# Optimization experiments

Hardware: AMD Instinct MI355X
Metric: run time of the kernel (lower is better)

## Reference

```python
import jax, jax.numpy as jnp
import numpy as np

N, E = 200_000, 1_000_000
WIDTH, NUM_HEAD = 128, 8
WN, WA = 1, 1            # width_norm, width_act
C = WIDTH * WN           # pre/norm channels
A = WIDTH * WA           # gate/value channels
BOND_SIZE, BAG = 33, 3
EPS = 1e-5               # GroupNorm eps (torch default)


def group_norm(x, groups, eps=EPS):
    # x: [E, C]; normalize per sample per group (affine=False, spatial size 1)
    e, c = x.shape
    xg = x.reshape(e, groups, c // groups)
    m = xg.mean(-1, keepdims=True)
    v = ((xg - m) ** 2).mean(-1, keepdims=True)
    return ((xg - m) * jax.lax.rsqrt(v + eps)).reshape(e, c)


def grouped1x1(x, w, groups):
    # grouped Conv1d with kernel 1, no bias. x: [E, Cin], w: [Cout, Cin//groups]
    e, cin = x.shape
    cout = w.shape[0]
    xg = x.reshape(e, groups, cin // groups)
    wg = w.reshape(groups, cout // groups, cin // groups)
    return jnp.einsum('egi,goi->ego', xg, wg).reshape(e, cout)


def setup_inputs() -> dict:
    key = jax.random.key(0)
    ks = jax.random.split(key, 12)
    x = jax.random.normal(ks[0], (N, WIDTH), jnp.float32)
    # degrees clamped to >= 1 in the original model
    deg = jnp.floor(jax.random.uniform(ks[1], (N,), jnp.float32, 1.0, 8.0))
    edge_idx = jax.random.randint(ks[2], (2, E), 0, N)
    edge_attr = jax.random.randint(ks[3], (E, BAG), 0, BOND_SIZE)
    s_in = 1.0 / np.sqrt(WIDTH)
    s_g = 1.0 / np.sqrt(C // NUM_HEAD)
    s_p = 1.0 / np.sqrt(A)
    pre0_w = jax.random.normal(ks[4], (C, WIDTH), jnp.float32) * s_in
    pre0_b = jnp.zeros((C,), jnp.float32)
    pre1_w = jax.random.normal(ks[5], (C, WIDTH), jnp.float32) * s_in
    pre1_b = jnp.zeros((C,), jnp.float32)
    emb = jax.random.normal(ks[6], (BOND_SIZE, C), jnp.float32)
    emb = emb.at[0].set(0.0)  # padding_idx=0
    gate_w = jax.random.normal(ks[7], (A, C // NUM_HEAD), jnp.float32) * s_g
    value_w = jax.random.normal(ks[8], (A, C // NUM_HEAD), jnp.float32) * s_g
    post_w = jax.random.normal(ks[9], (WIDTH, A), jnp.float32) * s_p
    post_b = jnp.zeros((WIDTH,), jnp.float32)
    degree_param = jnp.full((WIDTH,), -0.01, jnp.float32)
    return {"x": x, "deg": deg, "edge_idx": edge_idx, "edge_attr": edge_attr,
            "pre0_w": pre0_w, "pre0_b": pre0_b, "pre1_w": pre1_w, "pre1_b": pre1_b,
            "emb": emb, "gate_w": gate_w, "value_w": value_w,
            "post_w": post_w, "post_b": post_b, "degree_param": degree_param}


def reference(x, deg, edge_idx, edge_attr, pre0_w, pre0_b, pre1_w, pre1_b,
              emb, gate_w, value_w, post_w, post_b, degree_param):
    n = x.shape[0]
    # conv1x1 projections on nodes, then gather to edges
    h0 = x @ pre0_w.T + pre0_b                      # [N, C]
    h1 = x @ pre1_w.T + pre1_b                      # [N, C]
    xx = h0[edge_idx[0]] + h1[edge_idx[1]]          # [E, C]
    xx = group_norm(xx, NUM_HEAD)
    # EmbeddingBag mean with padding_idx=0 excluded from the mean
    mask = (edge_attr != 0)                          # [E, BAG]
    bag = (emb[edge_attr] * mask[..., None]).sum(1)  # [E, C]
    cnt = jnp.maximum(mask.sum(-1), 1).astype(xx.dtype)
    bag = bag / cnt[:, None]
    # GLU-style gate * value (Dropout is identity at eval)
    gate = jax.nn.relu(grouped1x1(xx + bag, gate_w, NUM_HEAD))  # [E, A]
    val = grouped1x1(xx, value_w, NUM_HEAD)                     # [E, A]
    xx = gate * val
    # scatter-sum back to destination nodes
    agg = jax.ops.segment_sum(xx, edge_idx[1], num_segments=n)  # [N, A]
    out = agg @ post_w.T + post_b                                # [N, WIDTH]
    out = jnp.power(deg[:, None], degree_param) * out
    return out
```

## Files before the change

### kernel.cpp

```cpp
#include <hip/hip_runtime.h>
#include <hip/hip_bf16.h>
#include <hip/hip_fp16.h>


typedef unsigned short u16;
typedef unsigned int   u32;

#define WIDTH 128

#define OFF_W0   0
#define OFF_B0   16384
#define OFF_W1   16512
#define OFF_B1   32896
#define OFF_EMB  33024
#define OFF_GW   37248
#define OFF_VW   39296
#define OFF_PW   41344
#define OFF_PB   57728
#define OFF_DP   57856
#define OFF_WGC  57984
#define OFF_WVC  74368
#define OFF_BGC  90752
#define OFF_BVC  90880
#define OFF_DEG  91008
#define ARENA_PAD 291072

typedef __attribute__((ext_vector_type(8))) short bf16x8;
typedef __attribute__((ext_vector_type(8))) _Float16 f16x8;
typedef __attribute__((ext_vector_type(4))) float f32x4;
typedef __attribute__((ext_vector_type(2))) __fp16 f16x2;

__device__ __forceinline__ float b2f(u16 u){ return __uint_as_float(((u32)u) << 16); }
__device__ __forceinline__ u16   f2b(float f){
  u32 u = __float_as_uint(f);
  u += 0x7fffu + ((u >> 16) & 1u);
  return (u16)(u >> 16);
}
__device__ __forceinline__ u16   f2h(float f){ return __half_as_ushort(__float2half(f)); }
__device__ __forceinline__ float h2f(u16 u){ return __half2float(__ushort_as_half(u)); }

__device__ __forceinline__ f16x2 u2h(u32 u){ union { u32 a; f16x2 b; } c; c.a = u; return c.b; }
__device__ __forceinline__ u32   h2u(f16x2 h){ union { f16x2 b; u32 a; } c; c.b = h; return c.a; }

__device__ __forceinline__ f16x2 pkhfma(f16x2 a, f16x2 b, f16x2 c){
#if __has_builtin(__builtin_elementwise_fma)
  return __builtin_elementwise_fma(a, b, c);
#else
  return a * b + c;
#endif
}

#define DPPADD(s, ctrl) {                                                  \
  const float _t = __uint_as_float((u32)__builtin_amdgcn_update_dpp(       \
      0, (int)__float_as_uint(s), (ctrl), 0xF, 0xF, true));                \
  (s) += _t; }

__device__ __forceinline__ bool is_fp32(const void* degsrc){
  return ((*(const u32*)degsrc) & 0xffffu) == 0u;
}

__device__ __forceinline__ bf16x8 cvt8(float4 a, float4 b){
  bf16x8 r;
  r[0]=(short)f2b(a.x); r[1]=(short)f2b(a.y); r[2]=(short)f2b(a.z); r[3]=(short)f2b(a.w);
  r[4]=(short)f2b(b.x); r[5]=(short)f2b(b.y); r[6]=(short)f2b(b.z); r[7]=(short)f2b(b.w);
  return r;
}
__device__ __forceinline__ f16x8 cvt8h(float4 a, float4 b){
  f16x8 r;
  r[0]=(_Float16)a.x; r[1]=(_Float16)a.y; r[2]=(_Float16)a.z; r[3]=(_Float16)a.w;
  r[4]=(_Float16)b.x; r[5]=(_Float16)b.y; r[6]=(_Float16)b.z; r[7]=(_Float16)b.w;
  return r;
}
__device__ __forceinline__ f16x8 cvtbh(bf16x8 v){
  f16x8 r;
  #pragma unroll
  for (int j = 0; j < 8; ++j) r[j] = (_Float16)b2f((u16)v[j]);
  return r;
}

__device__ __forceinline__ u16 cvt_one(const void* src, int j, bool f32){
  return f32 ? f2b(((const float*)src)[j]) : ((const u16*)src)[j];
}
__device__ __forceinline__ u16 cvt_one_h(const void* src, int j, bool f32){
  return f32 ? f2h(((const float*)src)[j]) : f2h(b2f(((const u16*)src)[j]));
}
__device__ __forceinline__ float read_f(const void* src, int j, bool f32){
  return f32 ? ((const float*)src)[j] : b2f(((const u16*)src)[j]);
}

__global__ void k_init_hist(const void* w0, const void* b0, const void* w1, const void* b1,
                            const void* emb, const void* gw, const void* vw,
                            const void* pw, const void* pb, const void* dp,
                            const void* degsrc, const int* __restrict__ eidx,
                            int* __restrict__ cnt, int E,
                            u16* __restrict__ pb16, u16* __restrict__ gembh,
                            float* __restrict__ gsums, int N)
{
  const bool f32 = is_fp32(degsrc);
  const int nbh = (E + 255) >> 8;
  const int tot_cvt = OFF_WGC + N;
  const int nbc = (tot_cvt + 255) >> 8;
  int b = blockIdx.x;
  const int t = threadIdx.x;

  if (b < nbh) {
    const int e = b * 256 + t;
    if (e < E) atomicAdd(&cnt[eidx[E + e]], 1);
    return;
  }
  b -= nbh;
  if (b < nbc) {
    const int i = b * 256 + t;
    if (i >= tot_cvt) return;
    u16 v; int dsti = i;
    if      (i < OFF_B0 ) v = cvt_one(w0,  i,           f32);
    else if (i < OFF_W1 ) v = cvt_one(b0,  i - OFF_B0,  f32);
    else if (i < OFF_B1 ) v = cvt_one(w1,  i - OFF_W1,  f32);
    else if (i < OFF_EMB) v = cvt_one(b1,  i - OFF_B1,  f32);
    else if (i < OFF_GW ) v = cvt_one(emb, i - OFF_EMB, f32);
    else if (i < OFF_VW ) v = cvt_one_h(gw, i - OFF_GW, f32);
    else if (i < OFF_PW ) v = cvt_one_h(vw, i - OFF_VW, f32);
    else if (i < OFF_PB ) v = cvt_one_h(pw, i - OFF_PW, f32);
    else if (i < OFF_DP ) v = cvt_one(pb,  i - OFF_PB,  f32);
    else if (i < OFF_WGC) v = cvt_one(dp,  i - OFF_DP,  f32);
    else { v = cvt_one(degsrc, i - OFF_WGC, f32); dsti = OFF_DEG + (i - OFF_WGC); }
    pb16[dsti] = v;
    return;
  }
  b -= nbc;
  if (b < 17) {
    const int tid = b * 256 + t;
    if (tid >= 33 * 128) return;
    const int a = tid >> 7, c = tid & 127, g = c >> 4;
    float s = 0.f;
    #pragma unroll
    for (int i = 0; i < 16; ++i)
      s += read_f(gw, c * 16 + i, f32) * read_f(emb, a * WIDTH + g * 16 + i, f32);
    gembh[tid] = f2h(s);
    return;
  }
  b -= 17;
  if (b < 1) {
    if (t < 256) {
      const int c = t & 127;
      const void* src = (t >> 7) ? vw : gw;
      float s = 0.f;
      #pragma unroll
      for (int i = 0; i < 16; ++i) s += read_f(src, c * 16 + i, f32);
      gsums[t] = s;
    }
    return;
  }
  b -= 1;
  if (b < 128) {
    const int tid = b * 256 + t;
    const int m = tid >> 14;
    const int o = (tid >> 7) & 127;
    const int i = tid & 127;
    const void* wsel = m ? vw : gw;
    const int hb = (o >> 4) * 16;
    float s = 0.f;
    #pragma unroll
    for (int j = 0; j < 16; ++j)
      s += read_f(wsel, o * 16 + j, f32) * read_f(w0, (size_t)(hb + j) * 128 + i, f32);
    pb16[(m ? OFF_WVC : OFF_WGC) + o * 128 + i] = f2h(s);
    return;
  }
  if (t < 256) {
    const int m = t >> 7, o = t & 127, hb = (o >> 4) * 16;
    const void* wsel = m ? vw : gw;
    float s = 0.f;
    #pragma unroll
    for (int j = 0; j < 16; ++j)
      s += read_f(wsel, o * 16 + j, f32) * read_f(b0, hb + j, f32);
    pb16[(m ? OFF_BVC : OFF_BGC) + o] = f2h(s);
  }
}

__global__ __launch_bounds__(512, 2) void k_pre_scan1(
    const void* __restrict__ x, const u16* __restrict__ pb16,
    u32* __restrict__ pk0ab, u32* __restrict__ uv0d, u32* __restrict__ h1d,
    const void* __restrict__ degsrc,
    const int* __restrict__ cnt, int* __restrict__ bsum, int n, int npre)
{
  if ((int)blockIdx.x >= npre) {
    const int t = threadIdx.x, b = (int)blockIdx.x - npre;
    const int i0 = b * 1024 + t * 2;
    int s = 0;
    if (i0     < n) s += cnt[i0];
    if (i0 + 1 < n) s += cnt[i0 + 1];
    __shared__ int sb[512];
    sb[t] = s; __syncthreads();
    for (int d = 256; d > 0; d >>= 1) { if (t < d) sb[t] += sb[t + d]; __syncthreads(); }
    if (t == 0) bsum[b] = sb[0];
    return;
  }

  const int t = threadIdx.x;
  const int lane = t & 63, lid = lane & 15, quad = lane >> 4;
  const int w = t >> 6, mat = w >> 1, c0 = (w & 1) * 64;
  const int node0 = blockIdx.x * 64;
  const bool f32 = is_fp32(degsrc);
  const bool hp16 = (mat == 1) || (mat == 2);

  const u16* wsrc; const u16* bsv;
  u32* outp; int slot = 0; bool pkmode = false;
  if      (mat == 0) { wsrc = pb16 + OFF_W0;  bsv = pb16 + OFF_B0;  outp = pk0ab; slot = 0; pkmode = true; }
  else if (mat == 1) { wsrc = pb16 + OFF_WGC; bsv = pb16 + OFF_BGC; outp = pk0ab; slot = 1; pkmode = true; }
  else if (mat == 2) { wsrc = pb16 + OFF_WVC; bsv = pb16 + OFF_BVC; outp = uv0d; }
  else               { wsrc = pb16 + OFF_W1;  bsv = pb16 + OFF_B1;  outp = h1d; }

  float bias[2][2];
  #pragma unroll
  for (int ntp = 0; ntp < 2; ++ntp)
    #pragma unroll
    for (int eo = 0; eo < 2; ++eo) {
      const u16 braw = bsv[c0 + ntp * 32 + 2 * lid + eo];
      bias[ntp][eo] = hp16 ? h2f(braw) : b2f(braw);
    }

  f32x4 acc[4][2][2];
  #pragma unroll
  for (int mt = 0; mt < 4; ++mt)
    #pragma unroll
    for (int ntp = 0; ntp < 2; ++ntp)
      #pragma unroll
      for (int eo = 0; eo < 2; ++eo)
        #pragma unroll
        for (int r = 0; r < 4; ++r) acc[mt][ntp][eo][r] = bias[ntp][eo];

  if (!hp16) {
    #pragma unroll
    for (int ks = 0; ks < 4; ++ks) {
      bf16x8 a[4], bb[2][2];
      #pragma unroll
      for (int ntp = 0; ntp < 2; ++ntp)
        #pragma unroll
        for (int eo = 0; eo < 2; ++eo)
          bb[ntp][eo] = *(const bf16x8*)(wsrc +
              (size_t)(c0 + ntp * 32 + 2 * lid + eo) * WIDTH + ks * 32 + quad * 8);
      if (f32) {
        #pragma unroll
        for (int mt = 0; mt < 4; ++mt) {
          const float4* xr = (const float4*)((const float*)x +
              (size_t)(node0 + mt * 16 + lid) * WIDTH + ks * 32 + quad * 8);
          a[mt] = cvt8(xr[0], xr[1]);
        }
      } else {
        #pragma unroll
        for (int mt = 0; mt < 4; ++mt)
          a[mt] = *(const bf16x8*)((const u16*)x +
              (size_t)(node0 + mt * 16 + lid) * WIDTH + ks * 32 + quad * 8);
      }
      #pragma unroll
      for (int mt = 0; mt < 4; ++mt)
        #pragma unroll
        for (int ntp = 0; ntp < 2; ++ntp)
          #pragma unroll
          for (int eo = 0; eo < 2; ++eo)
            acc[mt][ntp][eo] = __builtin_amdgcn_mfma_f32_16x16x32_bf16(
                a[mt], bb[ntp][eo], acc[mt][ntp][eo], 0, 0, 0);
    }
  } else {
    #pragma unroll
    for (int ks = 0; ks < 4; ++ks) {
      f16x8 a[4], bb[2][2];
      #pragma unroll
      for (int ntp = 0; ntp < 2; ++ntp)
        #pragma unroll
        for (int eo = 0; eo < 2; ++eo)
          bb[ntp][eo] = *(const f16x8*)(wsrc +
              (size_t)(c0 + ntp * 32 + 2 * lid + eo) * WIDTH + ks * 32 + quad * 8);
      if (f32) {
        #pragma unroll
        for (int mt = 0; mt < 4; ++mt) {
          const float4* xr = (const float4*)((const float*)x +
              (size_t)(node0 + mt * 16 + lid) * WIDTH + ks * 32 + quad * 8);
          a[mt] = cvt8h(xr[0], xr[1]);
        }
      } else {
        #pragma unroll
        for (int mt = 0; mt < 4; ++mt)
          a[mt] = cvtbh(*(const bf16x8*)((const u16*)x +
              (size_t)(node0 + mt * 16 + lid) * WIDTH + ks * 32 + quad * 8));
      }
      #pragma unroll
      for (int mt = 0; mt < 4; ++mt)
        #pragma unroll
        for (int ntp = 0; ntp < 2; ++ntp)
          #pragma unroll
          for (int eo = 0; eo < 2; ++eo)
            acc[mt][ntp][eo] = __builtin_amdgcn_mfma_f32_16x16x32_f16(
                a[mt], bb[ntp][eo], acc[mt][ntp][eo], 0, 0, 0);
    }
  }

  #pragma unroll
  for (int mt = 0; mt < 4; ++mt)
    #pragma unroll
    for (int r = 0; r < 4; ++r) {
      const int node = node0 + mt * 16 + quad * 4 + r;
      #pragma unroll
      for (int ntp = 0; ntp < 2; ++ntp) {
        const int p = (c0 >> 1) + ntp * 16 + lid;
        const u32 pk = h2u(__builtin_amdgcn_cvt_pkrtz(
            acc[mt][ntp][0][r], acc[mt][ntp][1][r]));
        if (pkmode) outp[(size_t)node * 128 + p * 2 + slot] = pk;
        else        outp[(size_t)node * 64 + p] = pk;
      }
    }
}

__global__ void k_scan3(const int* __restrict__ cnt, const int* __restrict__ bsum,
                        int* __restrict__ off, int n){
  const int t = threadIdx.x, b = blockIdx.x;
  __shared__ int sp[256];
  int pv = 0;
  for (int j = t; j < b; j += 256) pv += bsum[j];
  sp[t] = pv; __syncthreads();
  for (int d = 128; d > 0; d >>= 1) { if (t < d) sp[t] += sp[t + d]; __syncthreads(); }
  const int bpref = sp[0];

  const int i0 = b * 1024 + t * 4;
  int c[4];
  #pragma unroll
  for (int j = 0; j < 4; ++j) { int i = i0 + j; c[j] = (i < n) ? cnt[i] : 0; }
  int tsum = c[0] + c[1] + c[2] + c[3];
  __shared__ int sb[256];
  sb[t] = tsum; __syncthreads();
  for (int d = 1; d < 256; d <<= 1) {
    int x = (t >= d) ? sb[t - d] : 0;
    __syncthreads();
    sb[t] += x;
    __syncthreads();
  }
  int run = bpref + sb[t] - tsum;
  #pragma unroll
  for (int j = 0; j < 4; ++j) {
    int i = i0 + j;
    if (i < n) off[i] = run;
    run += c[j];
  }
}

__global__ void k_scatter(const int* __restrict__ eidx, const int* __restrict__ eattr,
                          int* __restrict__ off, uint2* __restrict__ sedge, int E){
  const int e = blockIdx.x * 256 + threadIdx.x;
  if (e >= E) return;
  const int dst = eidx[E + e];
  const int pos = atomicAdd(&off[dst], 1);
  const u32 a0 = (u32)eattr[e*3+0], a1 = (u32)eattr[e*3+1], a2 = (u32)eattr[e*3+2];
  u32 cb = (a0 != 0) + (a1 != 0) + (a2 != 0);
  cb = cb ? cb : 1u;
  sedge[pos] = make_uint2((u32)eidx[e], a0 | (a1 << 6) | (a2 << 12) | (cb << 18));
}

__global__ __launch_bounds__(256, 6) void k_agg(
    const u32* __restrict__ pk32, const u32* __restrict__ uv32,
    const u16* __restrict__ h1, const uint2* __restrict__ sedge,
    const int* __restrict__ off, const u16* __restrict__ pb16,
    const u32* __restrict__ gembw, const float* __restrict__ gsums,
    u16* __restrict__ aggh, const int N)
{
  __shared__ u32 gl[2112];
  for (int j = threadIdx.x; j < 2112; j += 256) gl[j] = gembw[j];
  __syncthreads();

  const int base = ((blockIdx.x * 256 + threadIdx.x) >> 6) * 4;
  if (base >= N) return;
  const int q = threadIdx.x & 63;
  const int c0 = 2 * q;

  u32 gw0[8], gw1[8], vw0[8], vw1[8];
  {
    const u32* g = (const u32*)(pb16 + OFF_GW + (size_t)c0 * 16);
    const u32* v = (const u32*)(pb16 + OFF_VW + (size_t)c0 * 16);
    #pragma unroll
    for (int i = 0; i < 8; ++i) {
      gw0[i] = g[i]; gw1[i] = g[8 + i];
      vw0[i] = v[i]; vw1[i] = v[8 + i];
    }
  }
  const float gs0 = gsums[c0],       gs1 = gsums[c0 + 1];
  const float vs0 = gsums[128 + c0], vs1 = gsums[128 + c0 + 1];

  u32 h1w[4]; int nend[4];
  #pragma unroll
  for (int d = 0; d < 4; ++d) {
    const int dst = min(base + d, N - 1);
    h1w[d]  = *(const u32*)(h1 + (size_t)dst * WIDTH + c0);
    nend[d] = off[dst];
  }
  int ncur = base ? off[base - 1] : 0;
  const int nlast = nend[3];

  u32 hp = 0, ugp = 0, uvp = 0, g0w = 0, g1w = 0, g2w = 0; float pinv = 1.f;
  uint2 edn = make_uint2(0u, 0u);
  if (ncur < nlast) {
    const uint2 e0 = sedge[ncur];
    edn = sedge[min(ncur + 1, nlast - 1)];
    const u32 po = e0.x * 128u + (u32)(q * 2);
    hp  = pk32[po];
    ugp = pk32[po + 1];
    uvp = uv32[e0.x * 64u + (u32)q];
    const int a0 = e0.y & 63, a1 = (e0.y >> 6) & 63, a2 = (e0.y >> 12) & 63;
    g0w = gl[a0 * 64 + q];
    g1w = gl[a1 * 64 + q];
    g2w = gl[a2 * 64 + q];
    pinv = __builtin_amdgcn_rcpf((float)((e0.y >> 18) & 3));
  }

  #pragma unroll
  for (int d = 0; d < 4; ++d) {
    const f16x2 h1h = u2h(h1w[d]);

    f16x2 ag0 = u2h(0), ag1 = u2h(0), av0 = u2h(0), av1 = u2h(0);
#define DSTEP(J) {                                                             \
    const f16x2 xj = u2h((u32)__builtin_amdgcn_ds_swizzle(                     \
        (int)h1w[d], 0x18 | ((J) << 5)));                                      \
    ag0 = pkhfma(xj, u2h(gw0[J]), ag0);                                        \
    ag1 = pkhfma(xj, u2h(gw1[J]), ag1);                                        \
    av0 = pkhfma(xj, u2h(vw0[J]), av0);                                        \
    av1 = pkhfma(xj, u2h(vw1[J]), av1); }
    DSTEP(0) DSTEP(1) DSTEP(2) DSTEP(3) DSTEP(4) DSTEP(5) DSTEP(6) DSTEP(7)
#undef DSTEP
    const float ug1d0 = (float)ag0.x + (float)ag0.y;
    const float ug1d1 = (float)ag1.x + (float)ag1.y;
    const float uv1d0 = (float)av0.x + (float)av0.y;
    const float uv1d1 = (float)av1.x + (float)av1.y;

    const int n1 = nend[d];
    float acc0 = 0.f, acc1 = 0.f;

    for (int i = ncur; i < n1; ++i) {
      const u32 hp_c = hp, ug_c = ugp, uv_c = uvp;
      const u32 g0c = g0w, g1c = g1w, g2c = g2w;
      const float inv_c = pinv;
      {
        const uint2 en = edn;
        edn = sedge[min(i + 2, nlast - 1)];
        const u32 po = en.x * 128u + (u32)(q * 2);
        hp  = pk32[po];
        ugp = pk32[po + 1];
        uvp = uv32[en.x * 64u + (u32)q];
        const int a0 = en.y & 63, a1 = (en.y >> 6) & 63, a2 = (en.y >> 12) & 63;
        g0w = gl[a0 * 64 + q];
        g1w = gl[a1 * 64 + q];
        g2w = gl[a2 * 64 + q];
        pinv = __builtin_amdgcn_rcpf((float)((en.y >> 18) & 3));
      }

      const f16x2 xh = u2h(hp_c) + h1h;
      const float x0 = (float)xh.x, x1 = (float)xh.y;

      float s  = x0 + x1;
      float ss = fmaf(x0, x0, x1 * x1);
      DPPADD(s, 0xB1);  DPPADD(ss, 0xB1);
      DPPADD(s, 0x4E);  DPPADD(ss, 0x4E);
      DPPADD(s, 0x141); DPPADD(ss, 0x141);
      const float mean = s * 0.0625f;
      const float var  = fmaf(ss, 0.0625f, -mean * mean);
      const float rs   = __builtin_amdgcn_rsqf(var + 1e-5f);
      const float mrs  = mean * rs;

      const f16x2 bsum3 = u2h(g0c) + u2h(g1c) + u2h(g2c);
      const float bg0 = (float)bsum3.x * inv_c;
      const float bg1 = (float)bsum3.y * inv_c;

      const f16x2 ugh = u2h(ug_c), uvh = u2h(uv_c);
      const float gate0 = fmaf(rs, (float)ugh.x + ug1d0, fmaf(-mrs, gs0, bg0));
      const float gate1 = fmaf(rs, (float)ugh.y + ug1d1, fmaf(-mrs, gs1, bg1));
      const float val0  = fmaf(rs, (float)uvh.x + uv1d0, -mrs * vs0);
      const float val1  = fmaf(rs, (float)uvh.y + uv1d1, -mrs * vs1);
      acc0 = fmaf(fmaxf(gate0, 0.f), val0, acc0);
      acc1 = fmaf(fmaxf(gate1, 0.f), val1, acc1);
    }

    if (base + d < N)
      *(u32*)(aggh + (size_t)(base + d) * WIDTH + c0) =
          h2u(__builtin_amdgcn_cvt_pkrtz(acc0, acc1));
    ncur = n1;
  }
}

__global__ __launch_bounds__(256, 2) void k_post(
    const u16* __restrict__ aggh, const u16* __restrict__ pb16,
    void* __restrict__ out, const void* __restrict__ degsrc)
{
  const int t = threadIdx.x;
  const int lane = t & 63, lid = lane & 15, quad = lane >> 4;
  const int w = t >> 6, c0 = (w & 1) * 64, mh = (w >> 1) * 32;
  const int node0 = blockIdx.x * 64;
  const bool f32o = is_fp32(degsrc);

  f32x4 acc[2][4];
  float dpc[4];
  #pragma unroll
  for (int nt = 0; nt < 4; ++nt) {
    const float bias = b2f(pb16[OFF_PB + c0 + nt * 16 + lid]);
    dpc[nt] = b2f(pb16[OFF_DP + c0 + nt * 16 + lid]);
    #pragma unroll
    for (int mt = 0; mt < 2; ++mt)
      #pragma unroll
      for (int r = 0; r < 4; ++r) acc[mt][nt][r] = bias;
  }

  #pragma unroll
  for (int ks = 0; ks < 4; ++ks) {
    f16x8 a[2], b[4];
    #pragma unroll
    for (int nt = 0; nt < 4; ++nt)
      b[nt] = *(const f16x8*)(pb16 + OFF_PW + (size_t)(c0 + nt * 16 + lid) * WIDTH + ks * 32 + quad * 8);
    #pragma unroll
    for (int mt = 0; mt < 2; ++mt)
      a[mt] = *(const f16x8*)(aggh +
          (size_t)(node0 + mh + mt * 16 + lid) * WIDTH + ks * 32 + quad * 8);
    #pragma unroll
    for (int mt = 0; mt < 2; ++mt)
      #pragma unroll
      for (int nt = 0; nt < 4; ++nt)
        acc[mt][nt] = __builtin_amdgcn_mfma_f32_16x16x32_f16(a[mt], b[nt], acc[mt][nt], 0, 0, 0);
  }

  float logd[2][4];
  #pragma unroll
  for (int mt = 0; mt < 2; ++mt)
    #pragma unroll
    for (int r = 0; r < 4; ++r)
      logd[mt][r] = __logf(b2f(pb16[OFF_DEG + node0 + mh + mt * 16 + quad * 4 + r]));

  #pragma unroll
  for (int mt = 0; mt < 2; ++mt)
    #pragma unroll
    for (int nt = 0; nt < 4; ++nt)
      #pragma unroll
      for (int r = 0; r < 4; ++r) {
        const int node = node0 + mh + mt * 16 + quad * 4 + r;
        const float v = acc[mt][nt][r] * __expf(dpc[nt] * logd[mt][r]);
        if (f32o) ((float*)out)[(size_t)node * WIDTH + c0 + nt * 16 + lid] = v;
        else      ((u16*)out)[(size_t)node * WIDTH + c0 + nt * 16 + lid] = f2b(v);
      }
}

extern "C" void kernel_launch(void* const* d_in, const int* in_sizes, int n_in,
                              void* d_out, int out_size, void* d_ws, size_t ws_size,
                              hipStream_t stream)
{
  (void)n_in; (void)out_size; (void)ws_size;
  const void* x     = d_in[0];
  const void* deg   = d_in[1];
  const int*  eidx  = (const int*)d_in[2];
  const int*  eattr = (const int*)d_in[3];

  const int N = in_sizes[1];
  const int E = in_sizes[2] / 2;

  u16*   aggh = (u16*)d_ws;
  u16*   h1   = aggh + (size_t)N * WIDTH;
  u32*   pk0ab= (u32*)(h1 + (size_t)N * WIDTH);
  u16*   pb16 = (u16*)(pk0ab + (size_t)N * 128);
  u16*   gembh= pb16 + ARENA_PAD;
  float* gsums= (float*)(gembh + 33 * WIDTH);
  int*   cnt  = (int*)(gsums + 256);
  int*   off  = cnt + N;
  int*   bsum = off + N;
  uint2* sedge= (uint2*)(bsum + 1024);
  u32*   uv0d = (u32*)d_out;

  const int nbc = (OFF_WGC + N + 255) / 256;
  const int nbh = (E + 255) / 256;

  hipMemsetAsync(cnt, 0, (size_t)N * sizeof(int), stream);

  k_init_hist<<<nbh + nbc + 147, 256, 0, stream>>>(
      d_in[4], d_in[5], d_in[6], d_in[7], d_in[8], d_in[9], d_in[10],
      d_in[11], d_in[12], d_in[13], deg, eidx, cnt, E, pb16, gembh, gsums, N);

  const int npre = N / 64;
  const int nblk = (N + 1023) / 1024;
  k_pre_scan1<<<npre + nblk, 512, 0, stream>>>(
      x, pb16, pk0ab, uv0d, (u32*)h1, deg, cnt, bsum, N, npre);

  k_scan3  <<<nblk, 256, 0, stream>>>(cnt, bsum, off, N);
  k_scatter<<<nbh, 256, 0, stream>>>(eidx, eattr, off, sedge, E);

  k_agg<<<((size_t)N * 16 + 255) / 256, 256, 0, stream>>>(
      pk0ab, uv0d, h1, sedge, off, pb16, (const u32*)gembh, gsums, aggh, N);

  k_post<<<N / 64, 256, 0, stream>>>(aggh, pb16, d_out, deg);
}
```

Measured before the change: 668.4 us.

## Interleave source-node h0, gate and value projections; deepen edge prefetch to two

The three per-node fp16 projections used on the gather side (h0, gate-folded, value-folded) now sit together in one interleaved buffer with three words per channel pair, instead of a two-way packed buffer plus a separate value buffer. This is meant to pull all of a source node's gathered data from adjacent memory. The h1 buffer moves into the output buffer, which is reused as scratch. The aggregation loop now prefetches two edges ahead, holding two register sets, to hide gather latency. In exchange it uses more registers, and the stride-3 u32 layout is less aligned. A stray dead load statement was also added.

Measured after the change: 735.9 us. 1.1x slower.

```diff
diff --git a/kernel.cpp b/kernel.cpp
--- a/kernel.cpp
+++ b/kernel.cpp
@@ -179,7 +179,7 @@
 
 __global__ __launch_bounds__(512, 2) void k_pre_scan1(
     const void* __restrict__ x, const u16* __restrict__ pb16,
-    u32* __restrict__ pk0ab, u32* __restrict__ uv0d, u32* __restrict__ h1d,
+    u32* __restrict__ pk3, u32* __restrict__ h1d,
     const void* __restrict__ degsrc,
     const int* __restrict__ cnt, int* __restrict__ bsum, int n, int npre)
 {
@@ -204,10 +204,10 @@
   const bool hp16 = (mat == 1) || (mat == 2);
 
   const u16* wsrc; const u16* bsv;
-  u32* outp; int slot = 0; bool pkmode = false;
-  if      (mat == 0) { wsrc = pb16 + OFF_W0;  bsv = pb16 + OFF_B0;  outp = pk0ab; slot = 0; pkmode = true; }
-  else if (mat == 1) { wsrc = pb16 + OFF_WGC; bsv = pb16 + OFF_BGC; outp = pk0ab; slot = 1; pkmode = true; }
-  else if (mat == 2) { wsrc = pb16 + OFF_WVC; bsv = pb16 + OFF_BVC; outp = uv0d; }
+  u32* outp;
+  if      (mat == 0) { wsrc = pb16 + OFF_W0;  bsv = pb16 + OFF_B0;  outp = pk3; }
+  else if (mat == 1) { wsrc = pb16 + OFF_WGC; bsv = pb16 + OFF_BGC; outp = pk3; }
+  else if (mat == 2) { wsrc = pb16 + OFF_WVC; bsv = pb16 + OFF_BVC; outp = pk3; }
   else               { wsrc = pb16 + OFF_W1;  bsv = pb16 + OFF_B1;  outp = h1d; }
 
   float bias[2][2];
@@ -305,8 +305,9 @@
         const int p = (c0 >> 1) + ntp * 16 + lid;
         const u32 pk = h2u(__builtin_amdgcn_cvt_pkrtz(
             acc[mt][ntp][0][r], acc[mt][ntp][1][r]));
-        if (pkmode) outp[(size_t)node * 128 + p * 2 + slot] = pk;
-        else        outp[(size_t)node * 64 + p] = pk;
+        if (mat < 3) outp[(size_t)node * 192 + p * 3 + mat];
+        if (mat < 3) outp[(size_t)node * 192 + p * 3 + mat] = pk;
+        else         outp[(size_t)node * 64 + p] = pk;
       }
     }
 }
@@ -356,11 +357,10 @@
 }
 
 __global__ __launch_bounds__(256, 6) void k_agg(
-    const u32* __restrict__ pk32, const u32* __restrict__ uv32,
-    const u16* __restrict__ h1, const uint2* __restrict__ sedge,
-    const int* __restrict__ off, const u16* __restrict__ pb16,
-    const u32* __restrict__ gembw, const float* __restrict__ gsums,
-    u16* __restrict__ aggh, const int N)
+    const u32* __restrict__ pk3, const u32* __restrict__ h1d,
+    const uint2* __restrict__ sedge, const int* __restrict__ off,
+    const u16* __restrict__ pb16, const u32* __restrict__ gembw,
+    const float* __restrict__ gsums, u16* __restrict__ aggh, const int N)
 {
   __shared__ u32 gl[2112];
   for (int j = threadIdx.x; j < 2112; j += 256) gl[j] = gembw[j];
@@ -388,26 +388,29 @@
   #pragma unroll
   for (int d = 0; d < 4; ++d) {
     const int dst = min(base + d, N - 1);
-    h1w[d]  = *(const u32*)(h1 + (size_t)dst * WIDTH + c0);
+    h1w[d]  = h1d[(size_t)dst * 64 + q];
     nend[d] = off[dst];
   }
   int ncur = base ? off[base - 1] : 0;
   const int nlast = nend[3];
 
-  u32 hp = 0, ugp = 0, uvp = 0, g0w = 0, g1w = 0, g2w = 0; float pinv = 1.f;
-  uint2 edn = make_uint2(0u, 0u);
+  u32 A_h = 0, A_g = 0, A_v = 0, A_g0 = 0, A_g1 = 0, A_g2 = 0; float A_inv = 1.f;
+  u32 B_h = 0, B_g = 0, B_v = 0, B_g0 = 0, B_g1 = 0, B_g2 = 0; float B_inv = 1.f;
+  uint2 edd = make_uint2(0u, 0u);
+
+#define LOADP(P, DSC) {                                                        \
+    const u32* pp = pk3 + (size_t)((DSC).x * 192u + (u32)(q * 3));             \
+    P##_h = pp[0]; P##_g = pp[1]; P##_v = pp[2];                               \
+    const int a0 = (DSC).y & 63, a1 = ((DSC).y >> 6) & 63, a2 = ((DSC).y >> 12) & 63; \
+    P##_g0 = gl[a0 * 64 + q]; P##_g1 = gl[a1 * 64 + q]; P##_g2 = gl[a2 * 64 + q]; \
+    P##_inv = __builtin_amdgcn_rcpf((float)(((DSC).y >> 18) & 3)); }
+
   if (ncur < nlast) {
-    const uint2 e0 = sedge[ncur];
-    edn = sedge[min(ncur + 1, nlast - 1)];
-    const u32 po = e0.x * 128u + (u32)(q * 2);
-    hp  = pk32[po];
-    ugp = pk32[po + 1];
-    uvp = uv32[e0.x * 64u + (u32)q];
-    const int a0 = e0.y & 63, a1 = (e0.y >> 6) & 63, a2 = (e0.y >> 12) & 63;
-    g0w = gl[a0 * 64 + q];
-    g1w = gl[a1 * 64 + q];
-    g2w = gl[a2 * 64 + q];
-    pinv = __builtin_amdgcn_rcpf((float)((e0.y >> 18) & 3));
+    const uint2 d0 = sedge[ncur];
+    const uint2 d1 = sedge[min(ncur + 1, nlast - 1)];
+    edd = sedge[min(ncur + 2, nlast - 1)];
+    LOADP(A, d0)
+    LOADP(B, d1)
   }
 
   #pragma unroll
@@ -433,21 +436,16 @@
     float acc0 = 0.f, acc1 = 0.f;
 
     for (int i = ncur; i < n1; ++i) {
-      const u32 hp_c = hp, ug_c = ugp, uv_c = uvp;
-      const u32 g0c = g0w, g1c = g1w, g2c = g2w;
-      const float inv_c = pinv;
+      const u32 hp_c = A_h, ug_c = A_g, uv_c = A_v;
+      const u32 g0c = A_g0, g1c = A_g1, g2c = A_g2;
+      const float inv_c = A_inv;
+
+      A_h = B_h; A_g = B_g; A_v = B_v;
+      A_g0 = B_g0; A_g1 = B_g1; A_g2 = B_g2; A_inv = B_inv;
       {
-        const uint2 en = edn;
-        edn = sedge[min(i + 2, nlast - 1)];
-        const u32 po = en.x * 128u + (u32)(q * 2);
-        hp  = pk32[po];
-        ugp = pk32[po + 1];
-        uvp = uv32[en.x * 64u + (u32)q];
-        const int a0 = en.y & 63, a1 = (en.y >> 6) & 63, a2 = (en.y >> 12) & 63;
-        g0w = gl[a0 * 64 + q];
-        g1w = gl[a1 * 64 + q];
-        g2w = gl[a2 * 64 + q];
-        pinv = __builtin_amdgcn_rcpf((float)((en.y >> 18) & 3));
+        const uint2 en = edd;
+        edd = sedge[min(i + 3, nlast - 1)];
+        LOADP(B, en)
       }
 
       const f16x2 xh = u2h(hp_c) + h1h;
@@ -481,6 +479,7 @@
           h2u(__builtin_amdgcn_cvt_pkrtz(acc0, acc1));
     ncur = n1;
   }
+#undef LOADP
 }
 
 __global__ __launch_bounds__(256, 2) void k_post(
@@ -556,16 +555,15 @@
   const int E = in_sizes[2] / 2;
 
   u16*   aggh = (u16*)d_ws;
-  u16*   h1   = aggh + (size_t)N * WIDTH;
-  u32*   pk0ab= (u32*)(h1 + (size_t)N * WIDTH);
-  u16*   pb16 = (u16*)(pk0ab + (size_t)N * 128);
+  u32*   pk3  = (u32*)(aggh + (size_t)N * WIDTH);
+  u16*   pb16 = (u16*)(pk3 + (size_t)N * 192);
   u16*   gembh= pb16 + ARENA_PAD;
   float* gsums= (float*)(gembh + 33 * WIDTH);
   int*   cnt  = (int*)(gsums + 256);
   int*   off  = cnt + N;
   int*   bsum = off + N;
   uint2* sedge= (uint2*)(bsum + 1024);
-  u32*   uv0d = (u32*)d_out;
+  u32*   h1d  = (u32*)d_out;
 
   const int nbc = (OFF_WGC + N + 255) / 256;
   const int nbh = (E + 255) / 256;
@@ -579,13 +577,13 @@
   const int npre = N / 64;
   const int nblk = (N + 1023) / 1024;
   k_pre_scan1<<<npre + nblk, 512, 0, stream>>>(
-      x, pb16, pk0ab, uv0d, (u32*)h1, deg, cnt, bsum, N, npre);
+      x, pb16, pk3, h1d, deg, cnt, bsum, N, npre);
 
   k_scan3  <<<nblk, 256, 0, stream>>>(cnt, bsum, off, N);
   k_scatter<<<nbh, 256, 0, stream>>>(eidx, eattr, off, sedge, E);
 
   k_agg<<<((size_t)N * 16 + 255) / 256, 256, 0, stream>>>(
-      pk0ab, uv0d, h1, sedge, off, pb16, (const u32*)gembh, gsums, aggh, N);
+      pk3, h1d, sedge, off, pb16, (const u32*)gembh, gsums, aggh, N);
 
   k_post<<<N / 64, 256, 0, stream>>>(aggh, pb16, d_out, deg);
 }
```
